# Performance work log

Measured on AMD Instinct MI355X. Metric: run time of the kernel, lower is better.

The kernel has to match this reference:

```python
import jax, jax.numpy as jnp
import numpy as np

ALPHA = 1.0
MIN_FEATURE_SIZE = 1.0
SC = 1e-12                      # stabilizer added to first derivatives
EPS_V_FLOOR = 1e-32 / 6.0       # torch.tensor(1e-32 ** 1 / 6) == 1e-32/6 (** binds tighter than /)


def _grad2d(phi, d):
    """Vectorized equivalent of numerical_gradient_2d: central differences in the
    interior, one-sided forward/backward differences at the boundaries."""
    gx = jnp.concatenate([
        (phi[1:2, :] - phi[0:1, :]) / d,           # forward diff at i == 0
        (phi[2:, :] - phi[:-2, :]) / (2.0 * d),    # central diff in interior
        (phi[-1:, :] - phi[-2:-1, :]) / d,         # backward diff at i == H-1
    ], axis=0)
    gy = jnp.concatenate([
        (phi[:, 1:2] - phi[:, 0:1]) / d,
        (phi[:, 2:] - phi[:, :-2]) / (2.0 * d),
        (phi[:, -1:] - phi[:, -2:-1]) / d,
    ], axis=1)
    return gx, gy


def setup_inputs() -> dict:
    key = jax.random.key(0)
    eps = jax.random.normal(key, (4096, 4096), dtype=jnp.float32)
    grid_size = jnp.asarray(0.05, dtype=jnp.float32)
    return {"eps": eps, "grid_size": grid_size}


def reference(eps, grid_size):
    # mirror the field along axis 1 (torch.cat((eps, eps.flip(1)), dim=1)) -> [H, 2W]
    eps = jnp.concatenate([eps, eps[:, ::-1]], axis=1)

    # ls_derivatives: first derivatives (+SC), then second derivatives of those
    eps_x, eps_y = _grad2d(eps, grid_size)
    eps_x = eps_x + SC
    eps_y = eps_y + SC
    eps_xx, eps_xy = _grad2d(eps_x, grid_size)
    _, eps_yy = _grad2d(eps_y, grid_size)

    pi_d = np.pi / (1.1 * MIN_FEATURE_SIZE)
    eps_v = jnp.maximum(jnp.sqrt(eps_x**2 + eps_y**2), EPS_V_FLOOR)
    k = (eps_x**2 * eps_yy - 2.0 * eps_x * eps_y * eps_xy + eps_y**2 * eps_xx) / eps_v**3
    curve_const = jnp.abs(k * jnp.arctan(eps_v / eps)) - pi_d
    return jnp.nansum(ALPHA * jnp.maximum(curve_const, 0.0) * grid_size**2)
```

## Files before the change

kernel.cpp:

```cpp
#include <hip/hip_runtime.h>
#include <math.h>


#define BLOCK_X 256
#define ROWS_PER 8
#define TILE_COLS (2 * BLOCK_X + 4)
#define TILE_F2   (TILE_COLS / 2)
#define TILE_H    (ROWS_PER + 4)

__device__ __forceinline__ float curve_pt(
    float nn, float nw, float n, float ne,
    float ww, float w, float c, float e, float ee,
    float sw, float s, float se, float ss,
    float rd2, float two_d)
{
    const float pi_d = 3.14159265358979323846f / 1.1f;
    const float u  = s - n;
    const float v  = e - w;
    const float U  = fmaf(-2.0f, c, ss + nn);
    const float V  = fmaf(-2.0f, c, ee + ww);
    const float X2 = 2.0f * ((se - ne) - (sw - nw));
    const float u2 = u * u, v2 = v * v, uv = u * v;
    float W = u2 * V;
    W = fmaf(v2, U, W);
    W = fmaf(-uv, X2, W);
    const float S  = u2 + v2;
    const float rsq = __builtin_amdgcn_rsqf(S);
    const float r3  = (rsq * rsq) * rsq;
    const float kk  = fabsf(W) * r3;
    const float ae  = fabsf(c);
    const float rc  = __builtin_amdgcn_rcpf(ae);
    const float sq  = S * rsq;
    const float q   = (rd2 * sq) * rc;
    const float iq  = (ae * rsq) * two_d;
    const bool  big = q > 1.0f;
    const float t   = big ? iq : q;
    const float s2  = t * t;
    float p = fmaf(s2, -0.01172120f, 0.05265332f);
    p = fmaf(s2, p, -0.11643287f);
    p = fmaf(s2, p,  0.19354346f);
    p = fmaf(s2, p, -0.33262347f);
    p = fmaf(s2, p,  0.99997726f);
    float at = p * t;
    at = big ? (1.57079632679f - at) : at;
    const float cc = fmaf(kk * rd2, at, -pi_d);
    return fmaxf(cc, 0.0f);
}

__device__ float generic_rows(const float* __restrict__ eps, int Hn, int Wn,
                              int i0, int j, float rd)
{
    const float rd2 = 0.5f * rd;
    const float SC = 1e-12f;
    const float FLOORV = (float)(1e-32 / 6.0);
    const float pi_d = 3.14159265358979323846f / 1.1f;

    const int jm  = (j > 0) ? j - 1 : 0;
    const int jmm = (j > 1) ? j - 2 : 0;
    const int jp = j + 1, jpp = j + 2;
    const int cjp  = (jp  < Wn) ? jp  : (2 * Wn - 1 - jp);
    const int cjpp = (jpp < Wn) ? jpp : (2 * Wn - 1 - jpp);
    const float syj = (j == 0)  ? rd : rd2;
    const float sym = (jm == 0) ? rd : rd2;
    const float syp = rd2;

    float acc = 0.0f;
    for (int r = 0; r < ROWS_PER; ++r) {
        const int i = i0 + r;
        if (i >= Hn) break;
        const int im  = (i > 0) ? i - 1 : 0;
        const int ip  = (i < Hn - 1) ? i + 1 : Hn - 1;
        const int imm = (im > 0) ? im - 1 : 0;
        const int ipp = (ip < Hn - 1) ? ip + 1 : Hn - 1;
        const float sxi = (i == 0 || i == Hn - 1) ? rd : rd2;
        const float sxm = (im == 0) ? rd : rd2;
        const float sxp = (ip == Hn - 1) ? rd : rd2;

        const float* rowc  = eps + (size_t)i   * (size_t)Wn;
        const float* rown  = eps + (size_t)im  * (size_t)Wn;
        const float* rows_ = eps + (size_t)ip  * (size_t)Wn;
        const float* rownn = eps + (size_t)imm * (size_t)Wn;
        const float* rowss = eps + (size_t)ipp * (size_t)Wn;

        const float e_c  = rowc[j];
        const float e_n  = rown[j],   e_s  = rows_[j];
        const float e_nn = rownn[j],  e_ss = rowss[j];
        const float e_w  = rowc[jm],  e_e  = rowc[cjp];
        const float e_ww = rowc[jmm], e_ee = rowc[cjpp];
        const float e_nw = rown[jm],  e_ne = rown[cjp];
        const float e_sw = rows_[jm], e_se = rows_[cjp];

        const float ex = fmaf(e_s - e_n, sxi, SC);
        const float ey = fmaf(e_e - e_w, syj, SC);
        float exn = fmaf(e_c - e_nn, sxm, SC);
        float exs = fmaf(e_ss - e_c, sxp, SC);
        if (i == 0)      exn = ex;
        if (i == Hn - 1) exs = ex;
        const float exx = (exs - exn) * sxi;
        float eyw = fmaf(e_c - e_ww, sym, SC);
        const float eye = fmaf(e_ee - e_c, syp, SC);
        if (j == 0) eyw = ey;
        const float eyy = (eye - eyw) * syj;
        const float exy = ((e_se - e_ne) - (e_sw - e_nw)) * (sxi * syj);

        const float t1 = ex * ex;
        const float t2 = ey * ey;
        float num = t1 * eyy;
        num = fmaf(t2, exx, num);
        num = fmaf(-2.0f * (ex * ey), exy, num);

        float ev = __builtin_amdgcn_sqrtf(t1 + t2);
        ev = fmaxf(ev, FLOORV);
        const float rv = __builtin_amdgcn_rcpf(ev);
        const float k  = num * (rv * rv) * rv;
        const float ae = fabsf(e_c);
        const float rc = __builtin_amdgcn_rcpf(ae);
        const float q  = ev * rc;
        const float iq = ae * rv;
        const bool  big = q > 1.0f;
        const float t  = big ? iq : q;
        const float s2 = t * t;
        float p = fmaf(s2, -0.01172120f, 0.05265332f);
        p = fmaf(s2, p, -0.11643287f);
        p = fmaf(s2, p,  0.19354346f);
        p = fmaf(s2, p, -0.33262347f);
        p = fmaf(s2, p,  0.99997726f);
        float at = p * t;
        at = big ? (1.57079632679f - at) : at;
        const float cc = fabsf(k) * at - pi_d;
        acc += fmaxf(cc, 0.0f);
    }
    return acc;
}

__global__ __launch_bounds__(BLOCK_X, 4) void curve_partial_kernel(
    const float* __restrict__ eps, const float* __restrict__ gs,
    double* __restrict__ partial, int Hn, int Wn)
{
    __shared__ float2 tile2[TILE_H * TILE_F2];
    const int tx = threadIdx.x;
    const int jb = blockIdx.x * (2 * BLOCK_X);
    const int i0 = blockIdx.y * ROWS_PER;
    const float d  = gs[0];
    const float rd = 1.0f / d;
    const float rd2 = 0.5f * rd;
    const float two_d = 2.0f * d;

    const int p0 = jb + 2 * tx;
    const int p1 = p0 + 1;

    const bool row_int = (i0 >= 2) && (i0 + ROWS_PER + 2 <= Hn);

    float accf = 0.0f;
    if (row_int) {
        const float* gbase = eps + (size_t)(i0 - 2) * (size_t)Wn;
        const bool cint = (jb >= 2) && (jb + 2 * BLOCK_X + 2 <= Wn);
        if (cint) {
            const float2* g2 = (const float2*)(gbase + (jb - 2));
            const size_t rs = (size_t)(Wn / 2);
            #pragma unroll
            for (int r = 0; r < TILE_H; ++r)
                tile2[r * TILE_F2 + tx] = g2[(size_t)r * rs + tx];
            if (tx < 2) {
                #pragma unroll
                for (int r = 0; r < TILE_H; ++r)
                    tile2[r * TILE_F2 + BLOCK_X + tx] = g2[(size_t)r * rs + BLOCK_X + tx];
            }
        } else {
            float* tf = (float*)tile2;
            int c0 = jb - 2 + 2 * tx, c1 = c0 + 1;
            c0 = (c0 < 0) ? 0 : ((c0 >= Wn) ? 2 * Wn - 1 - c0 : c0);
            c1 = (c1 < 0) ? 0 : ((c1 >= Wn) ? 2 * Wn - 1 - c1 : c1);
            #pragma unroll
            for (int r = 0; r < TILE_H; ++r) {
                tf[r * TILE_COLS + 2 * tx]     = gbase[(size_t)r * Wn + c0];
                tf[r * TILE_COLS + 2 * tx + 1] = gbase[(size_t)r * Wn + c1];
            }
            if (tx < 2) {
                int e0 = jb - 2 + 2 * (BLOCK_X + tx), e1 = e0 + 1;
                e0 = (e0 < 0) ? 0 : ((e0 >= Wn) ? 2 * Wn - 1 - e0 : e0);
                e1 = (e1 < 0) ? 0 : ((e1 >= Wn) ? 2 * Wn - 1 - e1 : e1);
                #pragma unroll
                for (int r = 0; r < TILE_H; ++r) {
                    tf[r * TILE_COLS + 2 * (BLOCK_X + tx)]     = gbase[(size_t)r * Wn + e0];
                    tf[r * TILE_COLS + 2 * (BLOCK_X + tx) + 1] = gbase[(size_t)r * Wn + e1];
                }
            }
        }
        __syncthreads();

        if (p0 >= 2 && p1 < Wn) {
            const float2* t2 = tile2;
            const int b = tx;
            #pragma unroll
            for (int r = 0; r < ROWS_PER; ++r) {
                const float2 A  = t2[(r + 0) * TILE_F2 + b + 1];
                const float2 B0 = t2[(r + 1) * TILE_F2 + b    ];
                const float2 B1 = t2[(r + 1) * TILE_F2 + b + 1];
                const float2 B2 = t2[(r + 1) * TILE_F2 + b + 2];
                const float2 C0 = t2[(r + 2) * TILE_F2 + b    ];
                const float2 C1 = t2[(r + 2) * TILE_F2 + b + 1];
                const float2 C2 = t2[(r + 2) * TILE_F2 + b + 2];
                const float2 D0 = t2[(r + 3) * TILE_F2 + b    ];
                const float2 D1 = t2[(r + 3) * TILE_F2 + b + 1];
                const float2 D2 = t2[(r + 3) * TILE_F2 + b + 2];
                const float2 E  = t2[(r + 4) * TILE_F2 + b + 1];
                accf += curve_pt(A.x, B0.y, B1.x, B1.y,
                                 C0.x, C0.y, C1.x, C1.y, C2.x,
                                 D0.y, D1.x, D1.y, E.x, rd2, two_d);
                accf += curve_pt(A.y, B1.x, B1.y, B2.x,
                                 C0.y, C1.x, C1.y, C2.x, C2.y,
                                 D1.x, D1.y, D2.x, E.y, rd2, two_d);
            }
        } else {
            if (p0 < Wn) accf += generic_rows(eps, Hn, Wn, i0, p0, rd);
            if (p1 < Wn) accf += generic_rows(eps, Hn, Wn, i0, p1, rd);
        }
    } else {
        if (p0 < Wn) accf += generic_rows(eps, Hn, Wn, i0, p0, rd);
        if (p1 < Wn) accf += generic_rows(eps, Hn, Wn, i0, p1, rd);
    }

    double acc = (double)accf;
    #pragma unroll
    for (int off = 32; off > 0; off >>= 1)
        acc += __shfl_down(acc, off, 64);
    __shared__ double ldsr[BLOCK_X / 64];
    const int lane = tx & 63, wv = tx >> 6;
    if (lane == 0) ldsr[wv] = acc;
    __syncthreads();
    if (tx == 0) {
        partial[blockIdx.y * gridDim.x + blockIdx.x] =
            ldsr[0] + ldsr[1] + ldsr[2] + ldsr[3];
    }
}

__global__ __launch_bounds__(256) void curve_finish_kernel(
    const double* __restrict__ partial, int n,
    const float* __restrict__ gs, float* __restrict__ out)
{
    const int tx = threadIdx.x;
    double acc = 0.0;
    for (int idx = tx; idx < n; idx += 256) acc += partial[idx];
    #pragma unroll
    for (int off = 32; off > 0; off >>= 1)
        acc += __shfl_down(acc, off, 64);
    __shared__ double lds[4];
    const int lane = tx & 63, wv = tx >> 6;
    if (lane == 0) lds[wv] = acc;
    __syncthreads();
    if (tx == 0) {
        const double d = (double)gs[0];
        out[0] = (float)((lds[0] + lds[1] + lds[2] + lds[3]) * 2.0 * d * d);
    }
}

extern "C" void kernel_launch(void* const* d_in, const int* in_sizes, int n_in,
                              void* d_out, int out_size, void* d_ws, size_t ws_size,
                              hipStream_t stream) {
    const float* eps = (const float*)d_in[0];
    const float* gs  = (const float*)d_in[1];
    float* out = (float*)d_out;

    const int n = in_sizes[0];
    int Wn = (int)(sqrt((double)n) + 0.5);
    int Hn = n / Wn;

    const int gx = (Wn + 2 * BLOCK_X - 1) / (2 * BLOCK_X);
    const int gy = (Hn + ROWS_PER - 1) / ROWS_PER;
    double* partial = (double*)d_ws;

    curve_partial_kernel<<<dim3(gx, gy), BLOCK_X, 0, stream>>>(eps, gs, partial, Hn, Wn);
    curve_finish_kernel<<<1, 256, 0, stream>>>(partial, gx * gy, gs, out);
}
```

Measured before the change: 124.8 us.

## Replace LDS tile staging with direct global float2 stencil loads

Drops the shared-memory tile and its barrier, so each thread reads its stencil neighbours straight from global memory as float2 loads and relies on L1/L2 caches for reuse. Each loop iteration now produces two rows at once and shares the loaded neighbours between them. Rows per block double to 16 and the launch-bounds occupancy hint drops from 4 to 2. The cost is more global and cache load traffic and higher register pressure, traded against removing the LDS staging and the synchronisation.

```diff
diff --git a/kernel.cpp b/kernel.cpp
--- a/kernel.cpp
+++ b/kernel.cpp
@@ -3,10 +3,7 @@
 
 
 #define BLOCK_X 256
-#define ROWS_PER 8
-#define TILE_COLS (2 * BLOCK_X + 4)
-#define TILE_F2   (TILE_COLS / 2)
-#define TILE_H    (ROWS_PER + 4)
+#define ROWS_PER 16
 
 __device__ __forceinline__ float curve_pt(
     float nn, float nw, float n, float ne,
@@ -133,88 +130,63 @@
     return acc;
 }
 
-__global__ __launch_bounds__(BLOCK_X, 4) void curve_partial_kernel(
+__global__ __launch_bounds__(BLOCK_X, 2) void curve_partial_kernel(
     const float* __restrict__ eps, const float* __restrict__ gs,
     double* __restrict__ partial, int Hn, int Wn)
 {
-    __shared__ float2 tile2[TILE_H * TILE_F2];
     const int tx = threadIdx.x;
     const int jb = blockIdx.x * (2 * BLOCK_X);
+    const int p0 = jb + 2 * tx;
+    const int p1 = p0 + 1;
     const int i0 = blockIdx.y * ROWS_PER;
     const float d  = gs[0];
     const float rd = 1.0f / d;
     const float rd2 = 0.5f * rd;
     const float two_d = 2.0f * d;
 
-    const int p0 = jb + 2 * tx;
-    const int p1 = p0 + 1;
-
     const bool row_int = (i0 >= 2) && (i0 + ROWS_PER + 2 <= Hn);
+    const bool col_int = (p0 >= 2) && (p0 + 3 < Wn);
 
     float accf = 0.0f;
-    if (row_int) {
-        const float* gbase = eps + (size_t)(i0 - 2) * (size_t)Wn;
-        const bool cint = (jb >= 2) && (jb + 2 * BLOCK_X + 2 <= Wn);
-        if (cint) {
-            const float2* g2 = (const float2*)(gbase + (jb - 2));
-            const size_t rs = (size_t)(Wn / 2);
-            #pragma unroll
-            for (int r = 0; r < TILE_H; ++r)
-                tile2[r * TILE_F2 + tx] = g2[(size_t)r * rs + tx];
-            if (tx < 2) {
-                #pragma unroll
-                for (int r = 0; r < TILE_H; ++r)
-                    tile2[r * TILE_F2 + BLOCK_X + tx] = g2[(size_t)r * rs + BLOCK_X + tx];
-            }
-        } else {
-            float* tf = (float*)tile2;
-            int c0 = jb - 2 + 2 * tx, c1 = c0 + 1;
-            c0 = (c0 < 0) ? 0 : ((c0 >= Wn) ? 2 * Wn - 1 - c0 : c0);
-            c1 = (c1 < 0) ? 0 : ((c1 >= Wn) ? 2 * Wn - 1 - c1 : c1);
-            #pragma unroll
-            for (int r = 0; r < TILE_H; ++r) {
-                tf[r * TILE_COLS + 2 * tx]     = gbase[(size_t)r * Wn + c0];
-                tf[r * TILE_COLS + 2 * tx + 1] = gbase[(size_t)r * Wn + c1];
-            }
-            if (tx < 2) {
-                int e0 = jb - 2 + 2 * (BLOCK_X + tx), e1 = e0 + 1;
-                e0 = (e0 < 0) ? 0 : ((e0 >= Wn) ? 2 * Wn - 1 - e0 : e0);
-                e1 = (e1 < 0) ? 0 : ((e1 >= Wn) ? 2 * Wn - 1 - e1 : e1);
-                #pragma unroll
-                for (int r = 0; r < TILE_H; ++r) {
-                    tf[r * TILE_COLS + 2 * (BLOCK_X + tx)]     = gbase[(size_t)r * Wn + e0];
-                    tf[r * TILE_COLS + 2 * (BLOCK_X + tx) + 1] = gbase[(size_t)r * Wn + e1];
-                }
-            }
-        }
-        __syncthreads();
-
-        if (p0 >= 2 && p1 < Wn) {
-            const float2* t2 = tile2;
-            const int b = tx;
-            #pragma unroll
-            for (int r = 0; r < ROWS_PER; ++r) {
-                const float2 A  = t2[(r + 0) * TILE_F2 + b + 1];
-                const float2 B0 = t2[(r + 1) * TILE_F2 + b    ];
-                const float2 B1 = t2[(r + 1) * TILE_F2 + b + 1];
-                const float2 B2 = t2[(r + 1) * TILE_F2 + b + 2];
-                const float2 C0 = t2[(r + 2) * TILE_F2 + b    ];
-                const float2 C1 = t2[(r + 2) * TILE_F2 + b + 1];
-                const float2 C2 = t2[(r + 2) * TILE_F2 + b + 2];
-                const float2 D0 = t2[(r + 3) * TILE_F2 + b    ];
-                const float2 D1 = t2[(r + 3) * TILE_F2 + b + 1];
-                const float2 D2 = t2[(r + 3) * TILE_F2 + b + 2];
-                const float2 E  = t2[(r + 4) * TILE_F2 + b + 1];
-                accf += curve_pt(A.x, B0.y, B1.x, B1.y,
-                                 C0.x, C0.y, C1.x, C1.y, C2.x,
-                                 D0.y, D1.x, D1.y, E.x, rd2, two_d);
-                accf += curve_pt(A.y, B1.x, B1.y, B2.x,
-                                 C0.y, C1.x, C1.y, C2.x, C2.y,
-                                 D1.x, D1.y, D2.x, E.y, rd2, two_d);
-            }
-        } else {
-            if (p0 < Wn) accf += generic_rows(eps, Hn, Wn, i0, p0, rd);
-            if (p1 < Wn) accf += generic_rows(eps, Hn, Wn, i0, p1, rd);
+    if (row_int && col_int) {
+        const float* base = eps + (size_t)i0 * (size_t)Wn + p0;
+        const long   w    = (long)Wn;
+        #pragma unroll
+        for (int t = 0; t < ROWS_PER / 2; ++t) {
+            const float* r0  = base + (long)(2 * t) * w;
+            const float* rm2 = r0 - 2 * w;
+            const float* rm1 = r0 - w;
+            const float* rp1 = r0 + w;
+            const float* rp2 = r0 + 2 * w;
+            const float* rp3 = r0 + 3 * w;
+
+            const float2 T  = *(const float2*)(rm2);
+            const float2 N0 = *(const float2*)(rm1 - 2);
+            const float2 N1 = *(const float2*)(rm1);
+            const float2 N2 = *(const float2*)(rm1 + 2);
+            const float2 C0 = *(const float2*)(r0 - 2);
+            const float2 C1 = *(const float2*)(r0);
+            const float2 C2 = *(const float2*)(r0 + 2);
+            const float2 S0 = *(const float2*)(rp1 - 2);
+            const float2 S1 = *(const float2*)(rp1);
+            const float2 S2 = *(const float2*)(rp1 + 2);
+            const float2 U0 = *(const float2*)(rp2 - 2);
+            const float2 U1 = *(const float2*)(rp2);
+            const float2 U2 = *(const float2*)(rp2 + 2);
+            const float2 B  = *(const float2*)(rp3);
+
+            accf += curve_pt(T.x,  N0.y, N1.x, N1.y,
+                             C0.x, C0.y, C1.x, C1.y, C2.x,
+                             S0.y, S1.x, S1.y, U1.x, rd2, two_d);
+            accf += curve_pt(T.y,  N1.x, N1.y, N2.x,
+                             C0.y, C1.x, C1.y, C2.x, C2.y,
+                             S1.x, S1.y, S2.x, U1.y, rd2, two_d);
+            accf += curve_pt(N1.x, C0.y, C1.x, C1.y,
+                             S0.x, S0.y, S1.x, S1.y, S2.x,
+                             U0.y, U1.x, U1.y, B.x,  rd2, two_d);
+            accf += curve_pt(N1.y, C1.x, C1.y, C2.x,
+                             S0.y, S1.x, S1.y, S2.x, S2.y,
+                             U1.x, U1.y, U2.x, B.y,  rd2, two_d);
         }
     } else {
         if (p0 < Wn) accf += generic_rows(eps, Hn, Wn, i0, p0, rd);
```

Measured after the change: 146.9 us. 17.7% more time.
